# Performance work log

Hardware: AMD Instinct MI355X
Metric: run time of the kernel (lower is better)

The kernel has to match this reference:

```python
import jax, jax.numpy as jnp
import numpy as np

P_DROP = 0.3
TEMP = 1.0
UNC_THRESH = 0.3
TOP_K = 2
EXTRA_K = 2  # min(2, num_experts - top_k)
NUM_SAMPLES = 5


def setup_inputs() -> dict:
    key = jax.random.key(0)
    ks = jax.random.split(key, 7)
    B, D, H, E = 16384, 4096, 128, 64
    return {
        "x": jax.random.normal(ks[0], (B, D), jnp.float32),
        "W1": jax.random.normal(ks[1], (D, H), jnp.float32) / np.sqrt(D),
        "b1": jnp.zeros((H,), jnp.float32),
        "W2": jax.random.normal(ks[2], (H, E), jnp.float32) / np.sqrt(H),
        "b2": jnp.zeros((E,), jnp.float32),
        "mask1_u": jax.random.uniform(ks[3], (NUM_SAMPLES, B, H), jnp.float32),
        "mask2_u": jax.random.uniform(ks[4], (NUM_SAMPLES, B, E), jnp.float32),
    }


def reference(x, W1, b1, W2, b2, mask1_u, mask2_u):
    scale = 1.0 / (1.0 - P_DROP)
    # layer1: Linear -> ReLU -> Dropout; W1 is shared, so compute once and
    # apply per-sample dropout masks (identical math to the torch loop).
    h = jax.nn.relu(x @ W1 + b1)                              # [B, H]
    h = h[None] * ((mask1_u >= P_DROP).astype(h.dtype) * scale)  # [S, B, H]
    # layer2: Linear -> Dropout
    logits = jnp.einsum("sbh,he->sbe", h, W2) + b2            # [S, B, E]
    logits = logits * ((mask2_u >= P_DROP).astype(logits.dtype) * scale)

    mean_logits = logits.mean(axis=0)                          # [B, E]
    probs = jax.nn.softmax(mean_logits / TEMP, axis=-1)        # [B, E]
    all_probs = jax.nn.softmax(logits / TEMP, axis=-1)         # [S, B, E]
    # torch .std() is unbiased (ddof=1)
    uncertainty = jnp.std(all_probs, axis=0, ddof=1).mean(axis=-1)  # [B]

    # top_k + conditional expansion by EXTRA_K when uncertain.
    full_probs, full_idx = jax.lax.top_k(probs, TOP_K + EXTRA_K)
    topk_probs, topk_idx = full_probs[:, :TOP_K], full_idx[:, :TOP_K]
    uncertain = (uncertainty > UNC_THRESH)[:, None]
    extra_probs = jnp.where(uncertain, full_probs[:, TOP_K:], 0.0)
    extra_idx = jnp.where(uncertain, full_idx[:, TOP_K:], -1)
    out_idx = jnp.concatenate([topk_idx, extra_idx], axis=1)       # [B, TOP_K+EXTRA_K]
    out_probs = jnp.concatenate([topk_probs, extra_probs], axis=1)
    return out_idx, out_probs, uncertainty
```

## Files before the change

kernel.cpp:

```cpp
#include <hip/hip_runtime.h>

typedef short short8 __attribute__((ext_vector_type(8)));
typedef float f32x4 __attribute__((ext_vector_type(4)));

#define B_ROWS 16384
#define SCALE 1.4285714285714286f

__device__ __forceinline__ float bf2f(unsigned short u) {
    return __uint_as_float(((unsigned)u) << 16);
}
__device__ __forceinline__ unsigned short f2bf(float f) {
    unsigned u = __float_as_uint(f);
    u += 0x7fffu + ((u >> 16) & 1u);
    return (unsigned short)(u >> 16);
}

__device__ __forceinline__ void gl_lds16(const void* g, void* l) {
    __builtin_amdgcn_global_load_lds(
        (const __attribute__((address_space(1))) unsigned int*)g,
        (__attribute__((address_space(3))) unsigned int*)l, 16, 0, 0);
}

__device__ __forceinline__ float wave_max(float v) {
    #pragma unroll
    for (int m = 1; m < 64; m <<= 1) v = fmaxf(v, __shfl_xor(v, m, 64));
    return v;
}
__device__ __forceinline__ float wave_sum(float v) {
    #pragma unroll
    for (int m = 1; m < 64; m <<= 1) v += __shfl_xor(v, m, 64);
    return v;
}

__global__ void k_prep(const float* __restrict__ w1,
                       unsigned short* __restrict__ w1h,
                       unsigned short* __restrict__ w1l) {
    int tid = blockIdx.x * 256 + threadIdx.x;
    int n = tid >> 12, k = tid & 4095;
    float v = w1[k * 128 + n];
    unsigned short hi = f2bf(v);
    w1h[tid] = hi;
    w1l[tid] = f2bf(v - bf2f(hi));
}

__global__ __launch_bounds__(256) void k_gemm(const float* __restrict__ x,
                                              const unsigned short* __restrict__ w1h,
                                              const unsigned short* __restrict__ w1l,
                                              const float* __restrict__ b1,
                                              float* __restrict__ hout) {
    __shared__ unsigned short sAh[2][32 * 64], sAl[2][32 * 64];
    __shared__ unsigned short sBh[2][128 * 64], sBl[2][128 * 64];
    const int t = threadIdx.x;
    const int w = t >> 6, lane = t & 63;
    const int l15 = lane & 15, l4 = lane >> 4;
    const int rowBase = blockIdx.x << 5;

    f32x4 acc[2][2];
    #pragma unroll
    for (int i = 0; i < 2; ++i)
        #pragma unroll
        for (int j = 0; j < 2; ++j) {
            f32x4 z = {0.f, 0.f, 0.f, 0.f};
            acc[i][j] = z;
        }

    const int am = t >> 3, as = t & 7;
    const int apc = as ^ (am & 7);

    auto stage = [&](int buf, int k0) {
        #pragma unroll
        for (int j = 0; j < 4; ++j) {
            int c = j * 256 + t;
            int n = c >> 3;
            int cl = (c & 7) ^ (n & 7);
            const size_t go = (size_t)n * 4096 + k0 + (cl << 3);
            gl_lds16(w1h + go, &sBh[buf][c << 3]);
            gl_lds16(w1l + go, &sBl[buf][c << 3]);
        }
        const float* src = x + ((size_t)(rowBase + am) << 12) + k0 + (as << 3);
        float4 a0 = *(const float4*)src;
        float4 a1 = *(const float4*)(src + 4);
        float av[8] = {a0.x, a0.y, a0.z, a0.w, a1.x, a1.y, a1.z, a1.w};
        short8 H, L;
        #pragma unroll
        for (int i = 0; i < 8; ++i) {
            unsigned short hi = f2bf(av[i]);
            H[i] = (short)hi;
            L[i] = (short)f2bf(av[i] - bf2f(hi));
        }
        *(short8*)&sAh[buf][((am << 3) + apc) << 3] = H;
        *(short8*)&sAl[buf][((am << 3) + apc) << 3] = L;
    };

    stage(0, 0);
    __syncthreads();
    for (int it = 0; it < 64; ++it) {
        int buf = it & 1;
        if (it + 1 < 64) stage(buf ^ 1, (it + 1) << 6);
        #pragma unroll
        for (int ks = 0; ks < 2; ++ks) {
            short8 ah[2], al[2], bh[2], bl[2];
            #pragma unroll
            for (int mf = 0; mf < 2; ++mf) {
                int rm = (mf << 4) + l15;
                int pc = ((ks << 2) + l4) ^ (rm & 7);
                ah[mf] = *(const short8*)&sAh[buf][(((rm << 3) + pc)) << 3];
                al[mf] = *(const short8*)&sAl[buf][(((rm << 3) + pc)) << 3];
            }
            #pragma unroll
            for (int nf = 0; nf < 2; ++nf) {
                int rn = (w << 5) + (nf << 4) + l15;
                int pc = ((ks << 2) + l4) ^ (rn & 7);
                bh[nf] = *(const short8*)&sBh[buf][(((rn << 3) + pc)) << 3];
                bl[nf] = *(const short8*)&sBl[buf][(((rn << 3) + pc)) << 3];
            }
            #pragma unroll
            for (int mf = 0; mf < 2; ++mf)
                #pragma unroll
                for (int nf = 0; nf < 2; ++nf) {
                    acc[mf][nf] = __builtin_amdgcn_mfma_f32_16x16x32_bf16(
                        ah[mf], bh[nf], acc[mf][nf], 0, 0, 0);
                    acc[mf][nf] = __builtin_amdgcn_mfma_f32_16x16x32_bf16(
                        ah[mf], bl[nf], acc[mf][nf], 0, 0, 0);
                    acc[mf][nf] = __builtin_amdgcn_mfma_f32_16x16x32_bf16(
                        al[mf], bh[nf], acc[mf][nf], 0, 0, 0);
                }
        }
        __syncthreads();
    }

    #pragma unroll
    for (int nf = 0; nf < 2; ++nf) {
        int col = (w << 5) + (nf << 4) + l15;
        float bias = b1[col];
        #pragma unroll
        for (int mf = 0; mf < 2; ++mf) {
            int r0 = rowBase + (mf << 4) + (l4 << 2);
            #pragma unroll
            for (int rr = 0; rr < 4; ++rr) {
                float v = acc[mf][nf][rr] + bias;
                hout[(size_t)(r0 + rr) * 128 + col] = v > 0.f ? v : 0.f;
            }
        }
    }
}

__global__ __launch_bounds__(256) void k_logstats(const float* __restrict__ h,
                                                  const float* __restrict__ w2,
                                                  const float* __restrict__ b2,
                                                  const float* __restrict__ m1,
                                                  const float* __restrict__ m2,
                                                  float* __restrict__ out) {
    __shared__ float lgs[5 * 32 * 64];
    const int t = threadIdx.x;
    const int lr = t >> 3;
    const int eg = t & 7;
    const int e0 = eg << 3;
    const int rowBase = blockIdx.x << 5;
    const int row = rowBase + lr;

    float acc[5][8];
    #pragma unroll
    for (int s = 0; s < 5; ++s)
        #pragma unroll
        for (int e = 0; e < 8; ++e) acc[s][e] = 0.f;

    const float* hp = h + (size_t)row * 128;
    const size_t m1row = (size_t)row * 128;

    for (int k = 0; k < 128; k += 4) {
        float4 h4 = *(const float4*)(hp + k);
        float hv[4] = {h4.x, h4.y, h4.z, h4.w};
        float w2v[4][8];
        #pragma unroll
        for (int kk = 0; kk < 4; ++kk) {
            float4 wa = *(const float4*)(w2 + (k + kk) * 64 + e0);
            float4 wb = *(const float4*)(w2 + (k + kk) * 64 + e0 + 4);
            w2v[kk][0] = wa.x; w2v[kk][1] = wa.y; w2v[kk][2] = wa.z; w2v[kk][3] = wa.w;
            w2v[kk][4] = wb.x; w2v[kk][5] = wb.y; w2v[kk][6] = wb.z; w2v[kk][7] = wb.w;
        }
        #pragma unroll
        for (int s = 0; s < 5; ++s) {
            float4 mu = *(const float4*)(m1 + (size_t)s * B_ROWS * 128 + m1row + k);
            float hd[4];
            hd[0] = (mu.x >= 0.3f) ? hv[0] * SCALE : 0.f;
            hd[1] = (mu.y >= 0.3f) ? hv[1] * SCALE : 0.f;
            hd[2] = (mu.z >= 0.3f) ? hv[2] * SCALE : 0.f;
            hd[3] = (mu.w >= 0.3f) ? hv[3] * SCALE : 0.f;
            #pragma unroll
            for (int kk = 0; kk < 4; ++kk)
                #pragma unroll
                for (int e = 0; e < 8; ++e)
                    acc[s][e] += hd[kk] * w2v[kk][e];
        }
    }

    float4 ba = *(const float4*)(b2 + e0);
    float4 bb = *(const float4*)(b2 + e0 + 4);
    float bv[8] = {ba.x, ba.y, ba.z, ba.w, bb.x, bb.y, bb.z, bb.w};
    #pragma unroll
    for (int s = 0; s < 5; ++s) {
        const float* m2p = m2 + ((size_t)s * B_ROWS + row) * 64 + e0;
        float4 ma = *(const float4*)m2p;
        float4 mb = *(const float4*)(m2p + 4);
        float mk[8] = {ma.x, ma.y, ma.z, ma.w, mb.x, mb.y, mb.z, mb.w};
        float lv[8];
        #pragma unroll
        for (int e = 0; e < 8; ++e) {
            float v = acc[s][e] + bv[e];
            lv[e] = (mk[e] >= 0.3f) ? v * SCALE : 0.f;
        }
        float* dst = &lgs[((s << 5) + lr) * 64 + e0];
        *(float4*)dst = make_float4(lv[0], lv[1], lv[2], lv[3]);
        *(float4*)(dst + 4) = make_float4(lv[4], lv[5], lv[6], lv[7]);
    }
    __syncthreads();

    const int wv = t >> 6, lane = t & 63;
    for (int r8 = 0; r8 < 8; ++r8) {
        int r = (wv << 3) + r8;
        float l[5], p[5];
        #pragma unroll
        for (int s = 0; s < 5; ++s)
            l[s] = lgs[((s << 5) + r) * 64 + lane];

        float ml = ((((l[0] + l[1]) + l[2]) + l[3]) + l[4]) / 5.0f;

        #pragma unroll
        for (int s = 0; s < 5; ++s) {
            float mx = wave_max(l[s]);
            float ev = expf(l[s] - mx);
            float sm = wave_sum(ev);
            p[s] = ev / sm;
        }

        float mx = wave_max(ml);
        float ev = expf(ml - mx);
        float sm = wave_sum(ev);
        float prob = ev / sm;

        float mean = ((((p[0] + p[1]) + p[2]) + p[3]) + p[4]) / 5.0f;
        float var = 0.f;
        #pragma unroll
        for (int s = 0; s < 5; ++s) { float d = p[s] - mean; var += d * d; }
        float sd = sqrtf(var * 0.25f);
        float unc = wave_sum(sd) / 64.0f;

        float pv = prob;
        float vv[4]; int vi[4];
        #pragma unroll
        for (int t4 = 0; t4 < 4; ++t4) {
            float bvx = pv; int bi = lane;
            #pragma unroll
            for (int m = 1; m < 64; m <<= 1) {
                float ov = __shfl_xor(bvx, m, 64);
                int oi = __shfl_xor(bi, m, 64);
                if (ov > bvx || (ov == bvx && oi < bi)) { bvx = ov; bi = oi; }
            }
            vv[t4] = bvx; vi[t4] = bi;
            if (lane == bi) pv = -1.f;
        }

        if (lane == 0) {
            int grow = rowBase + r;
            bool ug = unc > 0.3f;
            float4 fi = make_float4((float)vi[0], (float)vi[1],
                                    ug ? (float)vi[2] : -1.f,
                                    ug ? (float)vi[3] : -1.f);
            *(float4*)(out + (size_t)grow * 4) = fi;
            float4 fp = make_float4(vv[0], vv[1],
                                    ug ? vv[2] : 0.f,
                                    ug ? vv[3] : 0.f);
            *(float4*)(out + 65536 + (size_t)grow * 4) = fp;
            out[131072 + grow] = unc;
        }
    }
}

extern "C" void kernel_launch(void* const* d_in, const int* in_sizes, int n_in,
                              void* d_out, int out_size, void* d_ws, size_t ws_size,
                              hipStream_t stream) {
    const float* x  = (const float*)d_in[0];
    const float* W1 = (const float*)d_in[1];
    const float* b1 = (const float*)d_in[2];
    const float* W2 = (const float*)d_in[3];
    const float* b2 = (const float*)d_in[4];
    const float* m1 = (const float*)d_in[5];
    const float* m2 = (const float*)d_in[6];
    float* out = (float*)d_out;
    char* ws = (char*)d_ws;

    unsigned short* w1h = (unsigned short*)ws;
    unsigned short* w1l = (unsigned short*)(ws + (1 << 20));
    float* h = (float*)(ws + (2 << 20));

    k_prep    <<<2048, 256, 0, stream>>>(W1, w1h, w1l);
    k_gemm    <<<512,  256, 0, stream>>>(x, w1h, w1l, b1, h);
    k_logstats<<<512,  256, 0, stream>>>(h, W2, b2, m1, m2, out);
}
```

Measured before the change: 494.8 us.

## Fuse layer-1 GEMM and logit/stat kernel into one 512-thread kernel

Merges the GEMM and the logits/statistics kernels into a single kernel that keeps the hidden activations in shared memory instead of writing them to and re-reading them from global memory. Blocks grow to 512 threads (8 waves, one 16-column N slice each), and the x tile load is split into a register prefetch that is converted and written to LDS after the MFMAs, which overlaps the global load with compute. Shared memory per block rises to 80 KB and is reused across phases, which limits occupancy. Per-thread work in the logits phase is halved.

```diff
diff --git a/kernel.cpp b/kernel.cpp
--- a/kernel.cpp
+++ b/kernel.cpp
@@ -1,6 +1,7 @@
 #include <hip/hip_runtime.h>
 
 typedef short short8 __attribute__((ext_vector_type(8)));
+typedef short short4v __attribute__((ext_vector_type(4)));
 typedef float f32x4 __attribute__((ext_vector_type(4)));
 
 #define B_ROWS 16384
@@ -43,145 +44,152 @@
     w1l[tid] = f2bf(v - bf2f(hi));
 }
 
-__global__ __launch_bounds__(256) void k_gemm(const float* __restrict__ x,
-                                              const unsigned short* __restrict__ w1h,
-                                              const unsigned short* __restrict__ w1l,
-                                              const float* __restrict__ b1,
-                                              float* __restrict__ hout) {
-    __shared__ unsigned short sAh[2][32 * 64], sAl[2][32 * 64];
-    __shared__ unsigned short sBh[2][128 * 64], sBl[2][128 * 64];
+__global__ __launch_bounds__(512, 4) void k_fused(
+        const float* __restrict__ x,
+        const unsigned short* __restrict__ w1h,
+        const unsigned short* __restrict__ w1l,
+        const float* __restrict__ b1,
+        const float* __restrict__ w2,
+        const float* __restrict__ b2,
+        const float* __restrict__ m1,
+        const float* __restrict__ m2,
+        float* __restrict__ out) {
+    __shared__ __attribute__((aligned(128))) char smem[81920];
+    unsigned short* sAh0 = (unsigned short*)smem;
+    unsigned short* sAl0 = (unsigned short*)(smem + 8192);
+    unsigned short* sBh0 = (unsigned short*)(smem + 16384);
+    unsigned short* sBl0 = (unsigned short*)(smem + 49152);
+    float* hbuf = (float*)smem;
+    float* lgs  = (float*)(smem + 16384);
+
     const int t = threadIdx.x;
     const int w = t >> 6, lane = t & 63;
     const int l15 = lane & 15, l4 = lane >> 4;
     const int rowBase = blockIdx.x << 5;
 
-    f32x4 acc[2][2];
+    const int am = t >> 4;
+    const int rem = t & 15;
+    const int aDst = (((am << 3) + ((rem >> 1) ^ (am & 7))) << 3) + ((rem & 1) << 2);
+
+    f32x4 acc[2];
     #pragma unroll
-    for (int i = 0; i < 2; ++i)
+    for (int mf = 0; mf < 2; ++mf) {
+        f32x4 z = {0.f, 0.f, 0.f, 0.f};
+        acc[mf] = z;
+    }
+
+    auto stageB = [&](int buf, int k0) {
         #pragma unroll
         for (int j = 0; j < 2; ++j) {
-            f32x4 z = {0.f, 0.f, 0.f, 0.f};
-            acc[i][j] = z;
-        }
-
-    const int am = t >> 3, as = t & 7;
-    const int apc = as ^ (am & 7);
-
-    auto stage = [&](int buf, int k0) {
-        #pragma unroll
-        for (int j = 0; j < 4; ++j) {
-            int c = j * 256 + t;
+            int c = (j << 9) + t;
             int n = c >> 3;
             int cl = (c & 7) ^ (n & 7);
             const size_t go = (size_t)n * 4096 + k0 + (cl << 3);
-            gl_lds16(w1h + go, &sBh[buf][c << 3]);
-            gl_lds16(w1l + go, &sBl[buf][c << 3]);
-        }
-        const float* src = x + ((size_t)(rowBase + am) << 12) + k0 + (as << 3);
-        float4 a0 = *(const float4*)src;
-        float4 a1 = *(const float4*)(src + 4);
-        float av[8] = {a0.x, a0.y, a0.z, a0.w, a1.x, a1.y, a1.z, a1.w};
-        short8 H, L;
-        #pragma unroll
-        for (int i = 0; i < 8; ++i) {
+            gl_lds16(w1h + go, sBh0 + (buf << 13) + (c << 3));
+            gl_lds16(w1l + go, sBl0 + (buf << 13) + (c << 3));
+        }
+    };
+    auto loadA = [&](int k0) {
+        return *(const float4*)(x + ((size_t)(rowBase + am) << 12) + k0 + (rem << 2));
+    };
+    auto writeA = [&](int buf, float4 a0) {
+        float av[4] = {a0.x, a0.y, a0.z, a0.w};
+        short4v H, L;
+        #pragma unroll
+        for (int i = 0; i < 4; ++i) {
             unsigned short hi = f2bf(av[i]);
             H[i] = (short)hi;
             L[i] = (short)f2bf(av[i] - bf2f(hi));
         }
-        *(short8*)&sAh[buf][((am << 3) + apc) << 3] = H;
-        *(short8*)&sAl[buf][((am << 3) + apc) << 3] = L;
+        *(short4v*)(sAh0 + (buf << 11) + aDst) = H;
+        *(short4v*)(sAl0 + (buf << 11) + aDst) = L;
     };
 
-    stage(0, 0);
+    stageB(0, 0);
+    writeA(0, loadA(0));
     __syncthreads();
+
     for (int it = 0; it < 64; ++it) {
-        int buf = it & 1;
-        if (it + 1 < 64) stage(buf ^ 1, (it + 1) << 6);
+        const int buf = it & 1;
+        const bool pf = (it + 1 < 64);
+        float4 aN = make_float4(0.f, 0.f, 0.f, 0.f);
+        if (pf) {
+            stageB(buf ^ 1, (it + 1) << 6);
+            aN = loadA((it + 1) << 6);
+        }
         #pragma unroll
         for (int ks = 0; ks < 2; ++ks) {
-            short8 ah[2], al[2], bh[2], bl[2];
+            short8 ah[2], al[2], bh, bl;
             #pragma unroll
             for (int mf = 0; mf < 2; ++mf) {
                 int rm = (mf << 4) + l15;
                 int pc = ((ks << 2) + l4) ^ (rm & 7);
-                ah[mf] = *(const short8*)&sAh[buf][(((rm << 3) + pc)) << 3];
-                al[mf] = *(const short8*)&sAl[buf][(((rm << 3) + pc)) << 3];
-            }
-            #pragma unroll
-            for (int nf = 0; nf < 2; ++nf) {
-                int rn = (w << 5) + (nf << 4) + l15;
+                int o = ((rm << 3) + pc) << 3;
+                ah[mf] = *(const short8*)(sAh0 + (buf << 11) + o);
+                al[mf] = *(const short8*)(sAl0 + (buf << 11) + o);
+            }
+            {
+                int rn = (w << 4) + l15;
                 int pc = ((ks << 2) + l4) ^ (rn & 7);
-                bh[nf] = *(const short8*)&sBh[buf][(((rn << 3) + pc)) << 3];
-                bl[nf] = *(const short8*)&sBl[buf][(((rn << 3) + pc)) << 3];
-            }
-            #pragma unroll
-            for (int mf = 0; mf < 2; ++mf)
-                #pragma unroll
-                for (int nf = 0; nf < 2; ++nf) {
-                    acc[mf][nf] = __builtin_amdgcn_mfma_f32_16x16x32_bf16(
-                        ah[mf], bh[nf], acc[mf][nf], 0, 0, 0);
-                    acc[mf][nf] = __builtin_amdgcn_mfma_f32_16x16x32_bf16(
-                        ah[mf], bl[nf], acc[mf][nf], 0, 0, 0);
-                    acc[mf][nf] = __builtin_amdgcn_mfma_f32_16x16x32_bf16(
-                        al[mf], bh[nf], acc[mf][nf], 0, 0, 0);
-                }
-        }
+                int o = ((rn << 3) + pc) << 3;
+                bh = *(const short8*)(sBh0 + (buf << 13) + o);
+                bl = *(const short8*)(sBl0 + (buf << 13) + o);
+            }
+            #pragma unroll
+            for (int mf = 0; mf < 2; ++mf) {
+                acc[mf] = __builtin_amdgcn_mfma_f32_16x16x32_bf16(ah[mf], bh, acc[mf], 0, 0, 0);
+                acc[mf] = __builtin_amdgcn_mfma_f32_16x16x32_bf16(ah[mf], bl, acc[mf], 0, 0, 0);
+                acc[mf] = __builtin_amdgcn_mfma_f32_16x16x32_bf16(al[mf], bh, acc[mf], 0, 0, 0);
+            }
+        }
+        if (pf) writeA(buf ^ 1, aN);
         __syncthreads();
     }
 
-    #pragma unroll
-    for (int nf = 0; nf < 2; ++nf) {
-        int col = (w << 5) + (nf << 4) + l15;
-        float bias = b1[col];
+    {
+        const int col = (w << 4) + l15;
+        const float bias = b1[col];
         #pragma unroll
         for (int mf = 0; mf < 2; ++mf) {
-            int r0 = rowBase + (mf << 4) + (l4 << 2);
+            const int rbase = (mf << 4) + (l4 << 2);
             #pragma unroll
             for (int rr = 0; rr < 4; ++rr) {
-                float v = acc[mf][nf][rr] + bias;
-                hout[(size_t)(r0 + rr) * 128 + col] = v > 0.f ? v : 0.f;
-            }
-        }
-    }
-}
-
-__global__ __launch_bounds__(256) void k_logstats(const float* __restrict__ h,
-                                                  const float* __restrict__ w2,
-                                                  const float* __restrict__ b2,
-                                                  const float* __restrict__ m1,
-                                                  const float* __restrict__ m2,
-                                                  float* __restrict__ out) {
-    __shared__ float lgs[5 * 32 * 64];
-    const int t = threadIdx.x;
-    const int lr = t >> 3;
-    const int eg = t & 7;
-    const int e0 = eg << 3;
-    const int rowBase = blockIdx.x << 5;
+                const int r = rbase + rr;
+                float v = acc[mf][rr] + bias;
+                v = v > 0.f ? v : 0.f;
+                hbuf[r * 128 + (col ^ ((r & 7) << 2))] = v;
+            }
+        }
+    }
+    __syncthreads();
+
+    const int lr = t >> 4;
+    const int eg = t & 15;
+    const int e0 = eg << 2;
     const int row = rowBase + lr;
-
-    float acc[5][8];
+    const int lsw = (lr & 7) << 2;
+
+    float acc2[5][4];
     #pragma unroll
     for (int s = 0; s < 5; ++s)
         #pragma unroll
-        for (int e = 0; e < 8; ++e) acc[s][e] = 0.f;
-
-    const float* hp = h + (size_t)row * 128;
-    const size_t m1row = (size_t)row * 128;
+        for (int e = 0; e < 4; ++e) acc2[s][e] = 0.f;
+
+    const float* hrow = hbuf + lr * 128;
+    const size_t m1row = ((size_t)row) << 7;
 
     for (int k = 0; k < 128; k += 4) {
-        float4 h4 = *(const float4*)(hp + k);
+        float4 h4 = *(const float4*)(hrow + (k ^ lsw));
         float hv[4] = {h4.x, h4.y, h4.z, h4.w};
-        float w2v[4][8];
+        float w2v[4][4];
         #pragma unroll
         for (int kk = 0; kk < 4; ++kk) {
-            float4 wa = *(const float4*)(w2 + (k + kk) * 64 + e0);
-            float4 wb = *(const float4*)(w2 + (k + kk) * 64 + e0 + 4);
+            float4 wa = *(const float4*)(w2 + ((k + kk) << 6) + e0);
             w2v[kk][0] = wa.x; w2v[kk][1] = wa.y; w2v[kk][2] = wa.z; w2v[kk][3] = wa.w;
-            w2v[kk][4] = wb.x; w2v[kk][5] = wb.y; w2v[kk][6] = wb.z; w2v[kk][7] = wb.w;
         }
         #pragma unroll
         for (int s = 0; s < 5; ++s) {
-            float4 mu = *(const float4*)(m1 + (size_t)s * B_ROWS * 128 + m1row + k);
+            float4 mu = *(const float4*)(m1 + (size_t)s * (B_ROWS * 128) + m1row + k);
             float hd[4];
             hd[0] = (mu.x >= 0.3f) ? hv[0] * SCALE : 0.f;
             hd[1] = (mu.y >= 0.3f) ? hv[1] * SCALE : 0.f;
@@ -190,35 +198,33 @@
             #pragma unroll
             for (int kk = 0; kk < 4; ++kk)
                 #pragma unroll
-                for (int e = 0; e < 8; ++e)
-                    acc[s][e] += hd[kk] * w2v[kk][e];
-        }
-    }
-
-    float4 ba = *(const float4*)(b2 + e0);
-    float4 bb = *(const float4*)(b2 + e0 + 4);
-    float bv[8] = {ba.x, ba.y, ba.z, ba.w, bb.x, bb.y, bb.z, bb.w};
-    #pragma unroll
-    for (int s = 0; s < 5; ++s) {
-        const float* m2p = m2 + ((size_t)s * B_ROWS + row) * 64 + e0;
-        float4 ma = *(const float4*)m2p;
-        float4 mb = *(const float4*)(m2p + 4);
-        float mk[8] = {ma.x, ma.y, ma.z, ma.w, mb.x, mb.y, mb.z, mb.w};
-        float lv[8];
-        #pragma unroll
-        for (int e = 0; e < 8; ++e) {
-            float v = acc[s][e] + bv[e];
-            lv[e] = (mk[e] >= 0.3f) ? v * SCALE : 0.f;
-        }
-        float* dst = &lgs[((s << 5) + lr) * 64 + e0];
-        *(float4*)dst = make_float4(lv[0], lv[1], lv[2], lv[3]);
-        *(float4*)(dst + 4) = make_float4(lv[4], lv[5], lv[6], lv[7]);
+                for (int e = 0; e < 4; ++e)
+                    acc2[s][e] += hd[kk] * w2v[kk][e];
+        }
+    }
+
+    {
+        float4 ba = *(const float4*)(b2 + e0);
+        float bv4[4] = {ba.x, ba.y, ba.z, ba.w};
+        #pragma unroll
+        for (int s = 0; s < 5; ++s) {
+            const float* m2p = m2 + ((size_t)s * B_ROWS + row) * 64 + e0;
+            float4 ma = *(const float4*)m2p;
+            float mk[4] = {ma.x, ma.y, ma.z, ma.w};
+            float lv[4];
+            #pragma unroll
+            for (int e = 0; e < 4; ++e) {
+                float v = acc2[s][e] + bv4[e];
+                lv[e] = (mk[e] >= 0.3f) ? v * SCALE : 0.f;
+            }
+            *(float4*)(lgs + ((s << 5) + lr) * 64 + e0) =
+                make_float4(lv[0], lv[1], lv[2], lv[3]);
+        }
     }
     __syncthreads();
 
-    const int wv = t >> 6, lane = t & 63;
-    for (int r8 = 0; r8 < 8; ++r8) {
-        int r = (wv << 3) + r8;
+    for (int r4 = 0; r4 < 4; ++r4) {
+        const int r = (w << 2) + r4;
         float l[5], p[5];
         #pragma unroll
         for (int s = 0; s < 5; ++s)
@@ -249,7 +255,7 @@
         float pv = prob;
         float vv[4]; int vi[4];
         #pragma unroll
-        for (int t4 = 0; t4 < 4; ++t4) {
+        for (int q = 0; q < 4; ++q) {
             float bvx = pv; int bi = lane;
             #pragma unroll
             for (int m = 1; m < 64; m <<= 1) {
@@ -257,7 +263,7 @@
                 int oi = __shfl_xor(bi, m, 64);
                 if (ov > bvx || (ov == bvx && oi < bi)) { bvx = ov; bi = oi; }
             }
-            vv[t4] = bvx; vi[t4] = bi;
+            vv[q] = bvx; vi[q] = bi;
             if (lane == bi) pv = -1.f;
         }
 
@@ -292,9 +298,7 @@
 
     unsigned short* w1h = (unsigned short*)ws;
     unsigned short* w1l = (unsigned short*)(ws + (1 << 20));
-    float* h = (float*)(ws + (2 << 20));
-
-    k_prep    <<<2048, 256, 0, stream>>>(W1, w1h, w1l);
-    k_gemm    <<<512,  256, 0, stream>>>(x, w1h, w1l, b1, h);
-    k_logstats<<<512,  256, 0, stream>>>(h, W2, b2, m1, m2, out);
-}
+
+    k_prep <<<2048, 256, 0, stream>>>(W1, w1h, w1l);
+    k_fused<<<512,  512, 0, stream>>>(x, w1h, w1l, b1, W2, b2, m1, m2, out);
+}
```

Measured after the change: 484.0 us. 2.2% less time.
